# Performance work log

Measured on AMD Instinct MI355X. Metric: run time of the kernel, lower is better.

The kernel has to match this reference:

```python
import jax, jax.numpy as jnp
import numpy as np

B_, S, D_IN, D_OUT, R = 4, 2048, 4096, 4096, 64
SCALING = 16 / 64  # lora_alpha / r (use_rslora=False)


def setup_inputs() -> dict:
    key = jax.random.key(0)
    ks = jax.random.split(key, 7)
    return {
        "x": jax.random.normal(ks[0], (B_, S, D_IN), dtype=jnp.float32),
        "W_base": jax.random.normal(ks[1], (D_OUT, D_IN), dtype=jnp.float32) * 0.02,
        "b_base": jax.random.normal(ks[2], (D_OUT,), dtype=jnp.float32) * 0.02,
        "A": jax.random.normal(ks[3], (R, D_IN), dtype=jnp.float32) * 0.02,
        "B": jax.random.normal(ks[4], (D_OUT, R), dtype=jnp.float32) * 0.02,
        "WL": jax.random.normal(ks[5], (R, D_IN), dtype=jnp.float32) * 0.02,
        "WR": jax.random.normal(ks[6], (D_OUT, R), dtype=jnp.float32) * 0.02,
    }


def reference(x, W_base, b_base, A, B, WL, WR):
    # base linear: [b,s,in] @ [out,in]^T + bias
    result = jnp.einsum('bsi,oi->bso', x, W_base) + b_base
    # sparse_preserve_mode == 1:
    # result_A = lora_A(dropout(x)) + WL(x)   (dropout p=0 -> identity)
    a = jnp.einsum('bsi,ri->bsr', x, A) + jnp.einsum('bsi,ri->bsr', x, WL)
    # result_B = lora_B(result_A) + WR(result_A)
    b = jnp.einsum('bsr,or->bso', a, B) + jnp.einsum('bsr,or->bso', a, WR)
    return result + b * SCALING
```

## Files before the change

### kernel.cpp

```cpp
#include <hip/hip_runtime.h>
#include <hip/hip_bf16.h>

#define M_DIM 8192
#define N_DIM 4096
#define K_DIM 4096
#define R_DIM 64

typedef __attribute__((ext_vector_type(8))) short bf16x8;
typedef __attribute__((ext_vector_type(4))) float f32x4;

__device__ __forceinline__ ushort f2bf(float f) {
  union { float f; unsigned u; } v; v.f = f;
  unsigned r = v.u + 0x7fffu + ((v.u >> 16) & 1u);
  return (ushort)(r >> 16);
}

__device__ __forceinline__ void gload16(const void* g, void* l) {
  __builtin_amdgcn_global_load_lds(
      (const __attribute__((address_space(1))) void*)g,
      (__attribute__((address_space(3))) void*)l, 16, 0, 0);
}

__global__ void cvt_x_bf16(const float* __restrict__ x, ushort* __restrict__ xb, int n4) {
  int i = blockIdx.x * blockDim.x + threadIdx.x;
  int stride = gridDim.x * blockDim.x;
  const float4* x4 = (const float4*)x;
  ushort4* o4 = (ushort4*)xb;
  for (; i < n4; i += stride) {
    float4 v = x4[i];
    ushort4 o;
    o.x = f2bf(v.x); o.y = f2bf(v.y); o.z = f2bf(v.z); o.w = f2bf(v.w);
    o4[i] = o;
  }
}

__global__ void wcomb_bf16(const float* __restrict__ Wb, const float* __restrict__ lB,
                           const float* __restrict__ lWR, const float* __restrict__ lA,
                           const float* __restrict__ lWL, ushort* __restrict__ Wc) {
  __shared__ float BcT[64][65];
  __shared__ float Ac[64][64];
  const int t = threadIdx.x;
  const int ob = blockIdx.x >> 3;
  const int strip = blockIdx.x & 7;
  const int o0 = ob * 64;

#pragma unroll
  for (int e = 0; e < 16; ++e) {
    int idx = t + e * 256;
    int r = idx & 63, ol = idx >> 6;
    BcT[r][ol] = lB[(o0 + ol) * 64 + r] + lWR[(o0 + ol) * 64 + r];
  }

  const int to = (t & 15) * 4;
  const int ti = (t >> 4) * 4;

  for (int ic = 0; ic < 8; ++ic) {
    const int i0 = strip * 512 + ic * 64;
    __syncthreads();
#pragma unroll
    for (int e = 0; e < 16; ++e) {
      int idx = t + e * 256;
      int il = idx & 63, r = idx >> 6;
      Ac[r][il] = lA[r * 4096 + i0 + il] + lWL[r * 4096 + i0 + il];
    }
    __syncthreads();

    float acc[4][4] = {};
#pragma unroll 8
    for (int r = 0; r < 64; ++r) {
      float b0 = BcT[r][to], b1 = BcT[r][to + 1], b2 = BcT[r][to + 2], b3 = BcT[r][to + 3];
      float4 a4 = *(const float4*)&Ac[r][ti];
      acc[0][0] = fmaf(b0, a4.x, acc[0][0]); acc[0][1] = fmaf(b0, a4.y, acc[0][1]);
      acc[0][2] = fmaf(b0, a4.z, acc[0][2]); acc[0][3] = fmaf(b0, a4.w, acc[0][3]);
      acc[1][0] = fmaf(b1, a4.x, acc[1][0]); acc[1][1] = fmaf(b1, a4.y, acc[1][1]);
      acc[1][2] = fmaf(b1, a4.z, acc[1][2]); acc[1][3] = fmaf(b1, a4.w, acc[1][3]);
      acc[2][0] = fmaf(b2, a4.x, acc[2][0]); acc[2][1] = fmaf(b2, a4.y, acc[2][1]);
      acc[2][2] = fmaf(b2, a4.z, acc[2][2]); acc[2][3] = fmaf(b2, a4.w, acc[2][3]);
      acc[3][0] = fmaf(b3, a4.x, acc[3][0]); acc[3][1] = fmaf(b3, a4.y, acc[3][1]);
      acc[3][2] = fmaf(b3, a4.z, acc[3][2]); acc[3][3] = fmaf(b3, a4.w, acc[3][3]);
    }

#pragma unroll
    for (int oo = 0; oo < 4; ++oo) {
      size_t base = (size_t)(o0 + to + oo) * 4096 + i0 + ti;
      float4 wv = *(const float4*)&Wb[base];
      ushort4 ov;
      ov.x = f2bf(wv.x + 0.25f * acc[oo][0]);
      ov.y = f2bf(wv.y + 0.25f * acc[oo][1]);
      ov.z = f2bf(wv.z + 0.25f * acc[oo][2]);
      ov.w = f2bf(wv.w + 0.25f * acc[oo][3]);
      *(ushort4*)&Wc[base] = ov;
    }
  }
}

__global__ __launch_bounds__(256) void gemm_bt(const ushort* __restrict__ Xb,
                                               const ushort* __restrict__ Wc,
                                               const float* __restrict__ bias,
                                               float* __restrict__ out) {
  __shared__ ushort As[128 * 32];
  __shared__ ushort Bs[128 * 32];
  const int t = threadIdx.x;
  const int lane = t & 63;
  const int w = t >> 6;
  const int wr = w >> 1, wc = w & 1;
  const int bn = blockIdx.x & 31;
  const int bm = blockIdx.x >> 5;
  const int m0 = bm * 128, n0 = bn * 128;
  const int ln15 = lane & 15, k8 = (lane >> 4) * 8;

  const int srow = t >> 2, scol = (t & 3) * 8;
  const ushort* gA0 = Xb + (size_t)(m0 + srow) * K_DIM + scol;
  const ushort* gA1 = Xb + (size_t)(m0 + 64 + srow) * K_DIM + scol;
  const ushort* gB0 = Wc + (size_t)(n0 + srow) * K_DIM + scol;
  const ushort* gB1 = Wc + (size_t)(n0 + 64 + srow) * K_DIM + scol;

  f32x4 zero = {0.0f, 0.0f, 0.0f, 0.0f};
  f32x4 acc[4][4];
#pragma unroll
  for (int i = 0; i < 4; ++i)
#pragma unroll
    for (int j = 0; j < 4; ++j) acc[i][j] = zero;

  for (int kt = 0; kt < K_DIM / 32; ++kt) {
    const int kofs = kt * 32;
    gload16(gA0 + kofs, &As[t * 8]);
    gload16(gA1 + kofs, &As[2048 + t * 8]);
    gload16(gB0 + kofs, &Bs[t * 8]);
    gload16(gB1 + kofs, &Bs[2048 + t * 8]);
    __syncthreads();

    bf16x8 af[4], bfr[4];
#pragma unroll
    for (int f = 0; f < 4; ++f) {
      af[f] = *(const bf16x8*)&As[(wr * 64 + f * 16 + ln15) * 32 + k8];
      bfr[f] = *(const bf16x8*)&Bs[(wc * 64 + f * 16 + ln15) * 32 + k8];
    }
#pragma unroll
    for (int mf = 0; mf < 4; ++mf)
#pragma unroll
      for (int nf = 0; nf < 4; ++nf)
        acc[mf][nf] = __builtin_amdgcn_mfma_f32_16x16x32_bf16(af[mf], bfr[nf], acc[mf][nf], 0, 0, 0);
    __syncthreads();
  }

  const int rb = m0 + wr * 64 + (lane >> 4) * 4;
  const int cb = n0 + wc * 64 + ln15;
#pragma unroll
  for (int nf = 0; nf < 4; ++nf) {
    int col = cb + nf * 16;
    float bb = bias[col];
#pragma unroll
    for (int mf = 0; mf < 4; ++mf) {
#pragma unroll
      for (int j = 0; j < 4; ++j) {
        out[(size_t)(rb + mf * 16 + j) * N_DIM + col] = acc[mf][nf][j] + bb;
      }
    }
  }
}

extern "C" void kernel_launch(void* const* d_in, const int* in_sizes, int n_in,
                              void* d_out, int out_size, void* d_ws, size_t ws_size,
                              hipStream_t stream) {
  const float* x   = (const float*)d_in[0];
  const float* Wb  = (const float*)d_in[1];
  const float* bb  = (const float*)d_in[2];
  const float* lA  = (const float*)d_in[3];
  const float* lB  = (const float*)d_in[4];
  const float* lWL = (const float*)d_in[5];
  const float* lWR = (const float*)d_in[6];
  float* out = (float*)d_out;

  ushort* Xb = (ushort*)d_ws;
  ushort* Wc = (ushort*)((char*)d_ws + (size_t)M_DIM * K_DIM * 2);

  cvt_x_bf16<<<2048, 256, 0, stream>>>(x, Xb, M_DIM * K_DIM / 4);
  wcomb_bf16<<<512, 256, 0, stream>>>(Wb, lB, lWR, lA, lWL, Wc);
  gemm_bt<<<dim3(64 * 32), 256, 0, stream>>>(Xb, Wc, bb, out);
}
```

Measured before the change: 680.9 us.

## Rewrite GEMM with 256x256 tiles, 4-stage LDS pipeline, swizzle; merge prep kernels

```diff
diff --git a/kernel.cpp b/kernel.cpp
--- a/kernel.cpp
+++ b/kernel.cpp
@@ -4,7 +4,6 @@
 #define M_DIM 8192
 #define N_DIM 4096
 #define K_DIM 4096
-#define R_DIM 64
 
 typedef __attribute__((ext_vector_type(8))) short bf16x8;
 typedef __attribute__((ext_vector_type(4))) float f32x4;
@@ -21,27 +20,31 @@
       (__attribute__((address_space(3))) void*)l, 16, 0, 0);
 }
 
-__global__ void cvt_x_bf16(const float* __restrict__ x, ushort* __restrict__ xb, int n4) {
-  int i = blockIdx.x * blockDim.x + threadIdx.x;
-  int stride = gridDim.x * blockDim.x;
-  const float4* x4 = (const float4*)x;
-  ushort4* o4 = (ushort4*)xb;
-  for (; i < n4; i += stride) {
-    float4 v = x4[i];
-    ushort4 o;
-    o.x = f2bf(v.x); o.y = f2bf(v.y); o.z = f2bf(v.z); o.w = f2bf(v.w);
-    o4[i] = o;
-  }
-}
-
-__global__ void wcomb_bf16(const float* __restrict__ Wb, const float* __restrict__ lB,
-                           const float* __restrict__ lWR, const float* __restrict__ lA,
-                           const float* __restrict__ lWL, ushort* __restrict__ Wc) {
+__global__ void prep(const float* __restrict__ x, ushort* __restrict__ xb,
+                     const float* __restrict__ Wb, const float* __restrict__ lB,
+                     const float* __restrict__ lWR, const float* __restrict__ lA,
+                     const float* __restrict__ lWL, ushort* __restrict__ Wc) {
   __shared__ float BcT[64][65];
   __shared__ float Ac[64][64];
   const int t = threadIdx.x;
-  const int ob = blockIdx.x >> 3;
-  const int strip = blockIdx.x & 7;
+
+  if (blockIdx.x < 2048) {
+    int i = blockIdx.x * 256 + t;
+    const int n4 = M_DIM * K_DIM / 4;
+    const float4* x4 = (const float4*)x;
+    ushort4* o4 = (ushort4*)xb;
+    for (; i < n4; i += 2048 * 256) {
+      float4 v = x4[i];
+      ushort4 o;
+      o.x = f2bf(v.x); o.y = f2bf(v.y); o.z = f2bf(v.z); o.w = f2bf(v.w);
+      o4[i] = o;
+    }
+    return;
+  }
+
+  const int bid = blockIdx.x - 2048;
+  const int ob = bid >> 3;
+  const int strip = bid & 7;
   const int o0 = ob * 64;
 
 #pragma unroll
@@ -94,67 +97,105 @@
   }
 }
 
-__global__ __launch_bounds__(256) void gemm_bt(const ushort* __restrict__ Xb,
-                                               const ushort* __restrict__ Wc,
-                                               const float* __restrict__ bias,
-                                               float* __restrict__ out) {
-  __shared__ ushort As[128 * 32];
-  __shared__ ushort Bs[128 * 32];
+__global__ __launch_bounds__(512, 2) void gemm256(const ushort* __restrict__ Xb,
+                                                  const ushort* __restrict__ Wc,
+                                                  const float* __restrict__ bias,
+                                                  float* __restrict__ out) {
+  __shared__ char smem[131072];
   const int t = threadIdx.x;
   const int lane = t & 63;
-  const int w = t >> 6;
-  const int wr = w >> 1, wc = w & 1;
-  const int bn = blockIdx.x & 31;
-  const int bm = blockIdx.x >> 5;
-  const int m0 = bm * 128, n0 = bn * 128;
-  const int ln15 = lane & 15, k8 = (lane >> 4) * 8;
-
-  const int srow = t >> 2, scol = (t & 3) * 8;
-  const ushort* gA0 = Xb + (size_t)(m0 + srow) * K_DIM + scol;
-  const ushort* gA1 = Xb + (size_t)(m0 + 64 + srow) * K_DIM + scol;
-  const ushort* gB0 = Wc + (size_t)(n0 + srow) * K_DIM + scol;
-  const ushort* gB1 = Wc + (size_t)(n0 + 64 + srow) * K_DIM + scol;
-
-  f32x4 zero = {0.0f, 0.0f, 0.0f, 0.0f};
-  f32x4 acc[4][4];
-#pragma unroll
-  for (int i = 0; i < 4; ++i)
+  const int wid = t >> 6;
+  const int wm = wid >> 2, wn = wid & 3;
+  const int ln15 = lane & 15;
+  const int hi16 = (lane >> 4) * 16;
+
+  const int swz = (blockIdx.x & 7) * 64 + (blockIdx.x >> 3);
+  const int bm = swz >> 4, bn = swz & 15;
+  const int m0 = bm * 256, n0 = bn * 256;
+
+  int offA[8], offB[4];
+  {
+    const int rbA = wm * 128 + ln15;
+    const int xa = ((rbA >> 1) & 3) << 4;
+#pragma unroll
+    for (int mf = 0; mf < 8; ++mf) offA[mf] = ((rbA + mf * 16) * 64 + hi16) ^ xa;
+    const int rbB = wn * 64 + ln15;
+    const int xb2 = ((rbB >> 1) & 3) << 4;
+#pragma unroll
+    for (int nf = 0; nf < 4; ++nf) offB[nf] = ((rbB + nf * 16) * 64 + hi16) ^ xb2;
+  }
+
+  const int d0 = t * 16, d1 = 8192 + t * 16;
+  const int s0 = d0 ^ (((d0 >> 7) & 3) << 4);
+  const int s1 = d1 ^ (((d1 >> 7) & 3) << 4);
+  const ushort* pA0 = Xb + (size_t)(m0 + (s0 >> 6)) * K_DIM + ((s0 & 63) >> 1);
+  const ushort* pA1 = Xb + (size_t)(m0 + (s1 >> 6)) * K_DIM + ((s1 & 63) >> 1);
+  const ushort* pB0 = Wc + (size_t)(n0 + (s0 >> 6)) * K_DIM + ((s0 & 63) >> 1);
+  const ushort* pB1 = Wc + (size_t)(n0 + (s1 >> 6)) * K_DIM + ((s1 & 63) >> 1);
+
+  f32x4 acc[8][4];
+  f32x4 zero = {0.f, 0.f, 0.f, 0.f};
+#pragma unroll
+  for (int i = 0; i < 8; ++i)
 #pragma unroll
     for (int j = 0; j < 4; ++j) acc[i][j] = zero;
 
-  for (int kt = 0; kt < K_DIM / 32; ++kt) {
-    const int kofs = kt * 32;
-    gload16(gA0 + kofs, &As[t * 8]);
-    gload16(gA1 + kofs, &As[2048 + t * 8]);
-    gload16(gB0 + kofs, &Bs[t * 8]);
-    gload16(gB1 + kofs, &Bs[2048 + t * 8]);
-    __syncthreads();
-
-    bf16x8 af[4], bfr[4];
-#pragma unroll
-    for (int f = 0; f < 4; ++f) {
-      af[f] = *(const bf16x8*)&As[(wr * 64 + f * 16 + ln15) * 32 + k8];
-      bfr[f] = *(const bf16x8*)&Bs[(wc * 64 + f * 16 + ln15) * 32 + k8];
-    }
-#pragma unroll
-    for (int mf = 0; mf < 4; ++mf)
-#pragma unroll
-      for (int nf = 0; nf < 4; ++nf)
-        acc[mf][nf] = __builtin_amdgcn_mfma_f32_16x16x32_bf16(af[mf], bfr[nf], acc[mf][nf], 0, 0, 0);
-    __syncthreads();
-  }
-
-  const int rb = m0 + wr * 64 + (lane >> 4) * 4;
-  const int cb = n0 + wc * 64 + ln15;
+#define STAGE(kt, c)                                         \
+  do {                                                       \
+    char* sb_ = smem + (c) * 32768;                          \
+    gload16(pA0 + (kt) * 32, sb_ + d0);                      \
+    gload16(pA1 + (kt) * 32, sb_ + d1);                      \
+    gload16(pB0 + (kt) * 32, sb_ + 16384 + d0);              \
+    gload16(pB1 + (kt) * 32, sb_ + 16384 + d1);              \
+  } while (0)
+
+  STAGE(0, 0); STAGE(1, 1); STAGE(2, 2);
+  asm volatile("s_waitcnt vmcnt(8)" ::: "memory");
+  __builtin_amdgcn_s_barrier();
+  __builtin_amdgcn_sched_barrier(0);
+
+#define ITER(kt, c)                                                             \
+  do {                                                                          \
+    if ((kt) + 3 < 128) STAGE((kt) + 3, ((c) + 3) & 3);                         \
+    const char* sA = smem + (c) * 32768;                                        \
+    const char* sB = sA + 16384;                                                \
+    bf16x8 af[8], bg[4];                                                        \
+    _Pragma("unroll") for (int mf = 0; mf < 8; ++mf)                            \
+        af[mf] = *(const bf16x8*)(sA + offA[mf]);                               \
+    _Pragma("unroll") for (int nf = 0; nf < 4; ++nf)                            \
+        bg[nf] = *(const bf16x8*)(sB + offB[nf]);                               \
+    __builtin_amdgcn_s_setprio(1);                                              \
+    _Pragma("unroll") for (int mf = 0; mf < 8; ++mf)                            \
+      _Pragma("unroll") for (int nf = 0; nf < 4; ++nf)                          \
+        acc[mf][nf] = __builtin_amdgcn_mfma_f32_16x16x32_bf16(                  \
+            af[mf], bg[nf], acc[mf][nf], 0, 0, 0);                              \
+    __builtin_amdgcn_s_setprio(0);                                              \
+    if ((kt) < 125) { asm volatile("s_waitcnt vmcnt(8)" ::: "memory"); }        \
+    else            { asm volatile("s_waitcnt vmcnt(0)" ::: "memory"); }        \
+    __builtin_amdgcn_s_barrier();                                               \
+    __builtin_amdgcn_sched_barrier(0);                                          \
+  } while (0)
+
+  for (int ktb = 0; ktb < 128; ktb += 4) {
+    ITER(ktb + 0, 0);
+    ITER(ktb + 1, 1);
+    ITER(ktb + 2, 2);
+    ITER(ktb + 3, 3);
+  }
+#undef ITER
+#undef STAGE
+
+  const int rb = m0 + wm * 128 + (lane >> 4) * 4;
+  const int cb = n0 + wn * 64 + ln15;
 #pragma unroll
   for (int nf = 0; nf < 4; ++nf) {
-    int col = cb + nf * 16;
-    float bb = bias[col];
-#pragma unroll
-    for (int mf = 0; mf < 4; ++mf) {
+    const int col = cb + nf * 16;
+    const float bbv = bias[col];
+#pragma unroll
+    for (int mf = 0; mf < 8; ++mf) {
 #pragma unroll
       for (int j = 0; j < 4; ++j) {
-        out[(size_t)(rb + mf * 16 + j) * N_DIM + col] = acc[mf][nf][j] + bb;
+        out[(size_t)(rb + mf * 16 + j) * N_DIM + col] = acc[mf][nf][j] + bbv;
       }
     }
   }
@@ -175,7 +216,6 @@
   ushort* Xb = (ushort*)d_ws;
   ushort* Wc = (ushort*)((char*)d_ws + (size_t)M_DIM * K_DIM * 2);
 
-  cvt_x_bf16<<<2048, 256, 0, stream>>>(x, Xb, M_DIM * K_DIM / 4);
-  wcomb_bf16<<<512, 256, 0, stream>>>(Wb, lB, lWR, lA, lWL, Wc);
-  gemm_bt<<<dim3(64 * 32), 256, 0, stream>>>(Xb, Wc, bb, out);
-}
+  prep<<<2560, 256, 0, stream>>>(x, Xb, Wb, lB, lWR, lA, lWL, Wc);
+  gemm256<<<512, 512, 0, stream>>>(Xb, Wc, bb, out);
+}
```

After: 606.2 us. 1.12x faster.
